# Performance work log

Hardware: AMD Instinct MI355X
Metric: run time of the kernel (lower is better)

The kernel has to match this reference:

```python
import jax, jax.numpy as jnp
import numpy as np

B, M, N = 4, 1024, 4096
DQ, DC, H, DH = 512, 512, 8, 64
D = H * DH
NEG = -10000000.0


def setup_inputs() -> dict:
    key = jax.random.key(0)
    ks = jax.random.split(key, 7)
    left = jax.random.normal(ks[0], (B, M, DQ), dtype=jnp.float32)
    right = jax.random.normal(ks[1], (B, N, DC), dtype=jnp.float32)
    mask = jax.random.randint(ks[2], (B, M, N), 0, 2).astype(bool)
    # learned params (torch Linear stores weight as (out,in); we store (in,out))
    Wq = jax.random.normal(ks[3], (DQ, D), dtype=jnp.float32) * (DQ ** -0.5)
    Wkv = jax.random.normal(ks[4], (DC, 2 * D), dtype=jnp.float32) * (DC ** -0.5)
    Wout = jax.random.normal(ks[5], (D, DQ), dtype=jnp.float32) * (D ** -0.5)
    bout = jax.random.normal(ks[6], (DQ,), dtype=jnp.float32) * 0.01
    return {"left": left, "right": right, "mask": mask,
            "Wq": Wq, "Wkv": Wkv, "Wout": Wout, "bout": bout}


def reference(left, right, mask, Wq, Wkv, Wout, bout):
    scale = DH ** -0.5
    q = left @ Wq                      # (B, M, D)
    kv = right @ Wkv                   # (B, N, 2D)
    k, v = jnp.split(kv, 2, axis=-1)   # (B, N, D) each
    q = q.reshape(B, M, H, DH).transpose(0, 2, 1, 3)  # (B, H, M, DH)
    k = k.reshape(B, N, H, DH).transpose(0, 2, 1, 3)  # (B, H, N, DH)
    v = v.reshape(B, N, H, DH).transpose(0, 2, 1, 3)  # (B, H, N, DH)
    sim = scale * jnp.einsum('bhmd,bhnd->bhmn', q, k)  # (B, H, M, N)
    sim = jnp.where(mask[:, None, :, :], sim, NEG)
    attn = jax.nn.softmax(sim, axis=-1)
    out = jnp.einsum('bhmn,bhnd->bhmd', attn, v)       # (B, H, M, DH)
    out = out.transpose(0, 2, 1, 3).reshape(B, M, D)
    return out @ Wout + bout           # (B, M, DQ)
```

## Files before the change

### kernel.cpp

```cpp
#include <hip/hip_runtime.h>

typedef _Float16 f16;
typedef __attribute__((ext_vector_type(8))) _Float16 half8;
typedef __attribute__((ext_vector_type(4))) _Float16 half4;
typedef __attribute__((ext_vector_type(4))) float floatx4;
typedef unsigned int uint32;

#define MFMA16(a, b, c) __builtin_amdgcn_mfma_f32_16x16x32_f16((a), (b), (c), 0, 0, 0)

constexpr int B_ = 4, M_ = 1024, N_ = 4096, DQ_ = 512, DC_ = 512, H_ = 8, DH_ = 64, D_ = 512;
constexpr int KP_ = 576;
constexpr int VP_ = 4224;
constexpr int NSPLIT = 4;
constexpr float SCL_ = 0.125f;

typedef __attribute__((address_space(1))) const void glds_g;
typedef __attribute__((address_space(3))) void glds_l;
__device__ __forceinline__ void g2lds16(const void* g, void* l) {
    __builtin_amdgcn_global_load_lds((glds_g*)g, (glds_l*)l, 16, 0, 0);
}

__device__ __forceinline__ void wtr_tile(const float* __restrict__ src, f16* __restrict__ dst,
                                         int Nout, int bx, int by, int tid) {
    __shared__ __align__(16) f16 Ts[64][72];
    const int n0 = bx * 64, k0 = by * 64;
    {
        int kr = tid >> 2, q4 = tid & 3;
        const float* sp = src + (size_t)(k0 + kr) * Nout + n0 + q4 * 16;
        float4 x0 = *(const float4*)(sp + 0), x1 = *(const float4*)(sp + 4);
        float4 x2 = *(const float4*)(sp + 8), x3 = *(const float4*)(sp + 12);
        half8 h0, h1;
        h0[0]=(f16)x0.x; h0[1]=(f16)x0.y; h0[2]=(f16)x0.z; h0[3]=(f16)x0.w;
        h0[4]=(f16)x1.x; h0[5]=(f16)x1.y; h0[6]=(f16)x1.z; h0[7]=(f16)x1.w;
        h1[0]=(f16)x2.x; h1[1]=(f16)x2.y; h1[2]=(f16)x2.z; h1[3]=(f16)x2.w;
        h1[4]=(f16)x3.x; h1[5]=(f16)x3.y; h1[6]=(f16)x3.z; h1[7]=(f16)x3.w;
        *(half8*)&Ts[kr][q4 * 16] = h0;
        *(half8*)&Ts[kr][q4 * 16 + 8] = h1;
    }
    __syncthreads();
    {
        int nr = tid >> 2, q = tid & 3;
        half8 h0, h1;
#pragma unroll
        for (int j = 0; j < 8; j++) { h0[j] = Ts[q * 16 + j][nr]; h1[j] = Ts[q * 16 + 8 + j][nr]; }
        f16* dp = dst + (size_t)(n0 + nr) * 512 + k0 + q * 16;
        *(half8*)(dp + 0) = h0;
        *(half8*)(dp + 8) = h1;
    }
}

__global__ __launch_bounds__(256)
void prep_k(const void* __restrict__ mask, uint32* __restrict__ bits,
            const float* __restrict__ left, f16* __restrict__ leftb,
            const float* __restrict__ right, f16* __restrict__ rightb,
            const float* __restrict__ Wq, f16* __restrict__ wqt,
            const float* __restrict__ Wkv, f16* __restrict__ wkvt,
            const float* __restrict__ Wout, f16* __restrict__ woutt) {
    const int blk = blockIdx.x, tid = threadIdx.x;
    if (blk < 4096) {
        __shared__ int s_bad;
        if (tid == 0) s_bad = 0;
        __syncthreads();
        const uint32* w = (const uint32*)mask + (size_t)blk * 1024;
        int bad = 0;
#pragma unroll
        for (int j = 0; j < 4; j++) bad |= (w[tid * 4 + j] & 0xFFFFFFFEu) != 0u;
        if (bad) s_bad = 1;
        __syncthreads();
        const bool bytes_mode = s_bad != 0;
        const size_t base = (size_t)blk * 4096;
        const int lane = tid & 63;
        for (int j = 0; j < 16; j++) {
            size_t e = base + j * 256 + tid;
            bool pred = bytes_mode ? (((const unsigned char*)mask)[e] != 0)
                                   : (((const int*)mask)[e] != 0);
            unsigned long long bal = __ballot(pred);
            if (lane == 0)       bits[e >> 5] = (uint32)bal;
            else if (lane == 32) bits[e >> 5] = (uint32)(bal >> 32);
        }
    } else if (blk < 6144) {
        int i = ((blk - 4096) * 256 + tid) * 4;
        float4 x = *(const float4*)(left + i);
        half4 h; h[0] = (f16)x.x; h[1] = (f16)x.y; h[2] = (f16)x.z; h[3] = (f16)x.w;
        *(half4*)(leftb + i) = h;
    } else if (blk < 14336) {
        int i = ((blk - 6144) * 256 + tid) * 4;
        float4 x = *(const float4*)(right + i);
        half4 h; h[0] = (f16)x.x; h[1] = (f16)x.y; h[2] = (f16)x.z; h[3] = (f16)x.w;
        *(half4*)(rightb + i) = h;
    } else if (blk < 14400) {
        int r = blk - 14336;
        wtr_tile(Wq, wqt, 512, r & 7, r >> 3, tid);
    } else if (blk < 14528) {
        int r = blk - 14400;
        wtr_tile(Wkv, wkvt, 1024, r & 15, r >> 4, tid);
    } else {
        int r = blk - 14528;
        wtr_tile(Wout, woutt, 512, r & 7, r >> 3, tid);
    }
}

__global__ __launch_bounds__(256)
void gemmqkv_k(const f16* __restrict__ leftb, const f16* __restrict__ wqt,
               const f16* __restrict__ rightb, const f16* __restrict__ wkvt,
               f16* __restrict__ qb, f16* __restrict__ kb, f16* __restrict__ vt) {
    __shared__ __align__(16) f16 As[128 * 64];
    __shared__ __align__(16) f16 Bs[128 * 64];
    const int blk = blockIdx.x, tid = threadIdx.x;
    const int lane = tid & 63, wave = tid >> 6;
    const int qd = lane >> 4, l16 = lane & 15;
    const int wm = wave >> 1, wn = wave & 1;

    int mode;
    const f16* A; const f16* Bt; size_t m0, n0;
    if (blk < 1024) {
        size_t rows = (size_t)(blk & 127) * 128, cols = (size_t)(blk >> 7) * 128;
        if (cols < 512) { mode = 0; A = rightb; m0 = rows; Bt = wkvt;   n0 = cols; }
        else            { mode = 1; A = wkvt;   m0 = cols; Bt = rightb; n0 = rows; }
    } else {
        int r = blk - 1024;
        mode = 2; A = leftb; Bt = wqt;
        m0 = (size_t)(r & 31) * 128; n0 = (size_t)(r >> 5) * 128;
    }

    size_t goff[4];
    f16 *la[4], *lb[4];
#pragma unroll
    for (int i = 0; i < 4; i++) {
        int c = i * 256 + wave * 64 + lane;
        int row = c >> 3, col8 = (c & 7) ^ (row & 7);
        goff[i] = (size_t)row * 512 + col8 * 8;
        la[i] = As + (size_t)(i * 256 + wave * 64) * 8;
        lb[i] = Bs + (size_t)(i * 256 + wave * 64) * 8;
    }
    const f16* Ab = A + m0 * 512;
    const f16* Bb = Bt + n0 * 512;

    floatx4 acc[4][4] = {};

    for (int k0 = 0; k0 < 512; k0 += 64) {
        __syncthreads();
#pragma unroll
        for (int i = 0; i < 4; i++) g2lds16(Ab + goff[i] + k0, la[i]);
#pragma unroll
        for (int i = 0; i < 4; i++) g2lds16(Bb + goff[i] + k0, lb[i]);
        __syncthreads();
#pragma unroll
        for (int kk = 0; kk < 2; kk++) {
            half8 a[4], b[4];
#pragma unroll
            for (int t = 0; t < 4; t++) {
                int rowa = wm * 64 + t * 16 + l16;
                int rowb = wn * 64 + t * 16 + l16;
                int pa8 = ((kk * 4 + qd) ^ (rowa & 7)) * 8;
                int pb8 = ((kk * 4 + qd) ^ (rowb & 7)) * 8;
                a[t] = *(const half8*)&As[rowa * 64 + pa8];
                b[t] = *(const half8*)&Bs[rowb * 64 + pb8];
            }
#pragma unroll
            for (int mt = 0; mt < 4; mt++)
#pragma unroll
                for (int nt = 0; nt < 4; nt++)
                    acc[mt][nt] = MFMA16(a[mt], b[nt], acc[mt][nt]);
        }
    }

#pragma unroll
    for (int mt = 0; mt < 4; mt++)
#pragma unroll
        for (int nt = 0; nt < 4; nt++)
#pragma unroll
            for (int r = 0; r < 4; r++) {
                size_t mi = m0 + wm * 64 + mt * 16 + qd * 4 + r;
                size_t ni = n0 + wn * 64 + nt * 16 + l16;
                float v = acc[mt][nt][r];
                if (mode == 2) {
                    qb[mi * 512 + ni] = (f16)v;
                } else if (mode == 0) {
                    kb[mi * KP_ + ni] = (f16)v;
                } else {
                    int dcol = (int)mi - 512;
                    int hh = dcol >> 6, dh = dcol & 63;
                    size_t bb = ni >> 12, nn = ni & 4095;
                    vt[((bb * H_ + hh) * (size_t)DH_ + dh) * VP_ + nn] = (f16)v;
                }
            }
}

__global__ __launch_bounds__(256)
void attn_k(const f16* __restrict__ Qb, const f16* __restrict__ Kb,
            const f16* __restrict__ Vt, const uint32* __restrict__ mb,
            float* __restrict__ Op, float* __restrict__ Lp) {
    const int tid = threadIdx.x;
    const int lane = tid & 63, wave = tid >> 6;
    const int qd = lane >> 4, l16 = lane & 15;
    const int bh = blockIdx.x, b = bh >> 3, h = bh & 7;
    const int z = blockIdx.z;
    constexpr int iters = N_ / (64 * NSPLIT);
    const int n_base = z * iters * 64;
    const int m_base = blockIdx.y * 128 + wave * 32;

    __shared__ __align__(16) f16 Ks[64][72];
    __shared__ __align__(16) f16 Vs[64][72];
    __shared__ __align__(16) f16 psh[4][32][72];

    const f16 scl = (f16)SCL_;
    half8 q[2][2];
#pragma unroll
    for (int f = 0; f < 2; f++) {
        const f16* qrow = Qb + ((size_t)(b * M_ + m_base + f * 16 + l16)) * D_ + h * DH_;
        q[f][0] = *(const half8*)(qrow + qd * 8);
        q[f][1] = *(const half8*)(qrow + 32 + qd * 8);
#pragma unroll
        for (int j = 0; j < 8; j++) { q[f][0][j] = q[f][0][j] * scl; q[f][1][j] = q[f][1][j] * scl; }
    }
    const half8 ONE = {(f16)1, (f16)1, (f16)1, (f16)1, (f16)1, (f16)1, (f16)1, (f16)1};

    floatx4 ot[2][4] = {};
    floatx4 ol[2] = {};
    const uint32* mbase = mb + ((size_t)(b * M_ + m_base)) * (N_ / 32);

    const int snr = tid >> 2, scc = tid & 3;
    const f16* kg = Kb + ((size_t)(b * N_) + snr) * KP_ + h * DH_ + scc * 8;
    const f16* vg = Vt + ((size_t)bh * DH_ + snr) * VP_ + scc * 8;

    for (int it = 0; it < iters; it++) {
        const int n0 = n_base + it * 64;
        half8 kc0 = *(const half8*)(kg + (size_t)n0 * KP_);
        half8 kc1 = *(const half8*)(kg + (size_t)n0 * KP_ + 32);
        half8 vc0 = *(const half8*)(vg + n0);
        half8 vc1 = *(const half8*)(vg + n0 + 32);
        __syncthreads();
        *(half8*)&Ks[snr][scc * 8]      = kc0;
        *(half8*)&Ks[snr][32 + scc * 8] = kc1;
        *(half8*)&Vs[snr][scc * 8]      = vc0;
        *(half8*)&Vs[snr][32 + scc * 8] = vc1;
        __syncthreads();

        const int wi = n0 >> 5;
        uint32 msk[2][4][2];
#pragma unroll
        for (int f = 0; f < 2; f++)
#pragma unroll
            for (int r = 0; r < 4; r++) {
                const uint32* mr = mbase + (size_t)(f * 16 + qd * 4 + r) * (N_ / 32);
                uint2 mm = *(const uint2*)(mr + wi);
                msk[f][r][0] = mm.x >> l16;
                msk[f][r][1] = mm.y >> l16;
            }

#pragma unroll
        for (int s = 0; s < 4; s++) {
            half8 k0 = *(const half8*)&Ks[s * 16 + l16][qd * 8];
            half8 k1 = *(const half8*)&Ks[s * 16 + l16][32 + qd * 8];
#pragma unroll
            for (int f = 0; f < 2; f++) {
                floatx4 t = {};
                t = MFMA16(q[f][0], k0, t);
                t = MFMA16(q[f][1], k1, t);
#pragma unroll
                for (int r = 0; r < 4; r++) {
                    uint32 bit = (msk[f][r][s >> 1] >> ((s & 1) * 16)) & 1u;
                    float e = __expf(t[r]);
                    e = bit ? e : 0.0f;
                    psh[wave][f * 16 + qd * 4 + r][s * 16 + l16] = (f16)e;
                }
            }
        }
        half8 pa[2][2];
#pragma unroll
        for (int f = 0; f < 2; f++) {
            pa[f][0] = *(const half8*)&psh[wave][f * 16 + l16][qd * 8];
            pa[f][1] = *(const half8*)&psh[wave][f * 16 + l16][32 + qd * 8];
        }
#pragma unroll
        for (int f = 0; f < 2; f++) {
            ol[f] = MFMA16(ONE, pa[f][0], ol[f]);
            ol[f] = MFMA16(ONE, pa[f][1], ol[f]);
        }
#pragma unroll
        for (int sd = 0; sd < 4; sd++) {
            half8 v0 = *(const half8*)&Vs[sd * 16 + l16][qd * 8];
            half8 v1 = *(const half8*)&Vs[sd * 16 + l16][32 + qd * 8];
#pragma unroll
            for (int f = 0; f < 2; f++) {
                ot[f][sd] = MFMA16(v0, pa[f][0], ot[f][sd]);
                ot[f][sd] = MFMA16(v1, pa[f][1], ot[f][sd]);
            }
        }
    }

#pragma unroll
    for (int f = 0; f < 2; f++) {
        size_t row = (size_t)(z * 32 + bh) * M_ + m_base + f * 16 + l16;
        float* op = Op + row * DH_ + qd * 4;
#pragma unroll
        for (int sd = 0; sd < 4; sd++)
            *(floatx4*)(op + sd * 16) = ot[f][sd];
        if (qd == 0) Lp[row] = ol[f][0];
    }
}

__global__ __launch_bounds__(256)
void comb_k(const float* __restrict__ Op, const float* __restrict__ Lp, f16* __restrict__ Ob) {
    int i = blockIdx.x * 256 + threadIdx.x;
    int d = i & 63, m = (i >> 6) & 1023, bh = i >> 16;
    float num = 0.f, den = 0.f;
#pragma unroll
    for (int s = 0; s < NSPLIT; s++) {
        size_t row = ((size_t)s * 32 + bh) * M_ + m;
        num += Op[row * DH_ + d];
        den += Lp[row];
    }
    int b = bh >> 3, h = bh & 7;
    Ob[((size_t)(b * M_ + m)) * D_ + h * DH_ + d] = (f16)(num / den);
}

__global__ __launch_bounds__(256)
void gemmout_k(const f16* __restrict__ A, const f16* __restrict__ Bt,
               float* __restrict__ Fout, const float* __restrict__ bias) {
    __shared__ __align__(16) f16 As[128 * 32];
    __shared__ __align__(16) f16 Bs[128 * 32];
    const int tid = threadIdx.x;
    const int lane = tid & 63, wave = tid >> 6;
    const int qd = lane >> 4, l16 = lane & 15;
    const int wm = wave >> 1, wn = wave & 1;
    const size_t m0 = (size_t)blockIdx.x * 128;
    const size_t n0 = (size_t)blockIdx.y * 128;

    const int c1 = wave * 64 + lane;
    const int c2 = 256 + c1;
    f16* la1 = As + (size_t)(wave * 64) * 8;
    f16* la2 = As + (size_t)(256 + wave * 64) * 8;
    f16* lb1 = Bs + (size_t)(wave * 64) * 8;
    f16* lb2 = Bs + (size_t)(256 + wave * 64) * 8;

    floatx4 acc[4][4] = {};

    for (int k0 = 0; k0 < 512; k0 += 32) {
        __syncthreads();
        g2lds16(A + (m0 + (c1 >> 2)) * 512 + k0 + (c1 & 3) * 8, la1);
        g2lds16(A + (m0 + (c2 >> 2)) * 512 + k0 + (c2 & 3) * 8, la2);
        g2lds16(Bt + (n0 + (c1 >> 2)) * 512 + k0 + (c1 & 3) * 8, lb1);
        g2lds16(Bt + (n0 + (c2 >> 2)) * 512 + k0 + (c2 & 3) * 8, lb2);
        __syncthreads();
        half8 a[4], b[4];
#pragma unroll
        for (int t = 0; t < 4; t++) {
            a[t] = *(const half8*)&As[(wm * 64 + t * 16 + l16) * 32 + qd * 8];
            b[t] = *(const half8*)&Bs[(wn * 64 + t * 16 + l16) * 32 + qd * 8];
        }
#pragma unroll
        for (int mt = 0; mt < 4; mt++)
#pragma unroll
            for (int nt = 0; nt < 4; nt++)
                acc[mt][nt] = MFMA16(a[mt], b[nt], acc[mt][nt]);
    }

#pragma unroll
    for (int mt = 0; mt < 4; mt++)
#pragma unroll
        for (int nt = 0; nt < 4; nt++)
#pragma unroll
            for (int r = 0; r < 4; r++) {
                size_t row = m0 + wm * 64 + mt * 16 + qd * 4 + r;
                size_t col = n0 + wn * 64 + nt * 16 + l16;
                Fout[row * 512 + col] = acc[mt][nt][r] + bias[col];
            }
}

extern "C" void kernel_launch(void* const* d_in, const int* in_sizes, int n_in,
                              void* d_out, int out_size, void* d_ws, size_t ws_size,
                              hipStream_t stream) {
    const float* left  = (const float*)d_in[0];
    const float* right = (const float*)d_in[1];
    const void*  mask  = d_in[2];
    const float* Wq    = (const float*)d_in[3];
    const float* Wkv   = (const float*)d_in[4];
    const float* Wout  = (const float*)d_in[5];
    const float* bout  = (const float*)d_in[6];

    char* ws = (char*)d_ws;
    size_t off = 0;
    auto take = [&](size_t bytes) { char* p = ws + off; off += (bytes + 255) & ~(size_t)255; return p; };
    uint32* mbits = (uint32*)take((size_t)B_ * M_ * N_ / 8);
    f16* woutt = (f16*)take((size_t)D_ * DQ_ * 2);
    f16* qb    = (f16*)take((size_t)B_ * M_ * D_ * 2);
    f16* kb    = (f16*)take((size_t)B_ * N_ * KP_ * 2);
    f16* vt    = (f16*)take((size_t)B_ * H_ * DH_ * VP_ * 2);
    f16* ob    = (f16*)take((size_t)B_ * M_ * D_ * 2);
    char* pool = (char*)take((size_t)34 * 1024 * 1024);
    f16* leftb  = (f16*)pool;
    f16* rightb = (f16*)(pool + (size_t)4 * 1024 * 1024);
    f16* wqt    = (f16*)(pool + (size_t)20 * 1024 * 1024);
    f16* wkvt   = (f16*)(pool + (size_t)21 * 1024 * 1024);
    float* Op   = (float*)pool;
    float* Lp   = (float*)(pool + (size_t)NSPLIT * 32 * M_ * DH_ * 4);

    prep_k<<<14592, 256, 0, stream>>>(mask, mbits, left, leftb, right, rightb,
                                      Wq, wqt, Wkv, wkvt, Wout, woutt);
    gemmqkv_k<<<1152, 256, 0, stream>>>(leftb, wqt, rightb, wkvt, qb, kb, vt);
    attn_k<<<dim3(32, 8, NSPLIT), 256, 0, stream>>>(qb, kb, vt, mbits, Op, Lp);
    comb_k<<<8192, 256, 0, stream>>>(Op, Lp, ob);
    gemmout_k<<<dim3(32, 4), 256, 0, stream>>>(ob, woutt, (float*)d_out, bout);
}
```

Baseline: 281.5 us.

## Rework attention inner loop: direct LDS loads, register P transpose, exp2, more splits

K and V tiles now go straight from global memory into XOR-swizzled LDS through global_load_lds, which removes the register staging step. The QK^T MFMA operands are swapped so that each lane holds a row fragment. That fragment is then rebuilt into the PV operand with permlane32/16 swaps, so the per-wave P shared-memory round trip is gone. The softmax uses exp2 with log2(e) folded into the Q scale and packs results with cvt_pkrtz. The split count becomes 8 when the workspace is large enough, with an occupancy hint, and the combine kernel is vectorized to float4. This adds split-combine traffic, and permlane correctness depends on the lane layout.

```diff
diff --git a/kernel.cpp b/kernel.cpp
--- a/kernel.cpp
+++ b/kernel.cpp
@@ -5,14 +5,14 @@
 typedef __attribute__((ext_vector_type(4))) _Float16 half4;
 typedef __attribute__((ext_vector_type(4))) float floatx4;
 typedef unsigned int uint32;
+typedef __attribute__((ext_vector_type(4))) uint32 uint4v;
 
 #define MFMA16(a, b, c) __builtin_amdgcn_mfma_f32_16x16x32_f16((a), (b), (c), 0, 0, 0)
 
 constexpr int B_ = 4, M_ = 1024, N_ = 4096, DQ_ = 512, DC_ = 512, H_ = 8, DH_ = 64, D_ = 512;
 constexpr int KP_ = 576;
 constexpr int VP_ = 4224;
-constexpr int NSPLIT = 4;
-constexpr float SCL_ = 0.125f;
+constexpr float QSC_ = 0.18033688011112042f;
 
 typedef __attribute__((address_space(1))) const void glds_g;
 typedef __attribute__((address_space(3))) void glds_l;
@@ -187,7 +187,7 @@
             }
 }
 
-__global__ __launch_bounds__(256)
+__global__ __launch_bounds__(256, 6)
 void attn_k(const f16* __restrict__ Qb, const f16* __restrict__ Kb,
             const f16* __restrict__ Vt, const uint32* __restrict__ mb,
             float* __restrict__ Op, float* __restrict__ Lp) {
@@ -195,84 +195,102 @@
     const int lane = tid & 63, wave = tid >> 6;
     const int qd = lane >> 4, l16 = lane & 15;
     const int bh = blockIdx.x, b = bh >> 3, h = bh & 7;
-    const int z = blockIdx.z;
-    constexpr int iters = N_ / (64 * NSPLIT);
+    const int z = blockIdx.z, nsp = gridDim.z;
+    const int iters = N_ / (64 * nsp);
     const int n_base = z * iters * 64;
     const int m_base = blockIdx.y * 128 + wave * 32;
 
-    __shared__ __align__(16) f16 Ks[64][72];
-    __shared__ __align__(16) f16 Vs[64][72];
-    __shared__ __align__(16) f16 psh[4][32][72];
-
-    const f16 scl = (f16)SCL_;
+    __shared__ __align__(16) f16 Ks[64 * 64];
+    __shared__ __align__(16) f16 Vs[64 * 64];
+
     half8 q[2][2];
 #pragma unroll
     for (int f = 0; f < 2; f++) {
         const f16* qrow = Qb + ((size_t)(b * M_ + m_base + f * 16 + l16)) * D_ + h * DH_;
-        q[f][0] = *(const half8*)(qrow + qd * 8);
-        q[f][1] = *(const half8*)(qrow + 32 + qd * 8);
-#pragma unroll
-        for (int j = 0; j < 8; j++) { q[f][0][j] = q[f][0][j] * scl; q[f][1][j] = q[f][1][j] * scl; }
+        half8 r0 = *(const half8*)(qrow + qd * 8);
+        half8 r1 = *(const half8*)(qrow + 32 + qd * 8);
+#pragma unroll
+        for (int j = 0; j < 8; j++) {
+            q[f][0][j] = (f16)((float)r0[j] * QSC_);
+            q[f][1][j] = (f16)((float)r1[j] * QSC_);
+        }
     }
     const half8 ONE = {(f16)1, (f16)1, (f16)1, (f16)1, (f16)1, (f16)1, (f16)1, (f16)1};
 
     floatx4 ot[2][4] = {};
     floatx4 ol[2] = {};
-    const uint32* mbase = mb + ((size_t)(b * M_ + m_base)) * (N_ / 32);
-
-    const int snr = tid >> 2, scc = tid & 3;
-    const f16* kg = Kb + ((size_t)(b * N_) + snr) * KP_ + h * DH_ + scc * 8;
-    const f16* vg = Vt + ((size_t)bh * DH_ + snr) * VP_ + scc * 8;
+
+    const uint32* mrow0 = mb + ((size_t)(b * M_ + m_base + l16)) * (N_ / 32);
+    const uint32* mrow1 = mrow0 + (size_t)16 * (N_ / 32);
+
+    const int srow = wave * 16;
+    const int r8 = lane >> 3, p8 = lane & 7;
+    const int gc8 = p8 ^ r8;
+    const f16* kg = Kb + ((size_t)(b * N_) + srow + r8) * KP_ + h * DH_ + gc8 * 8;
+    const f16* vg = Vt + ((size_t)(bh * DH_) + srow + r8) * VP_ + gc8 * 8;
+    const int sw = (l16 & 7) * 8;
 
     for (int it = 0; it < iters; it++) {
         const int n0 = n_base + it * 64;
-        half8 kc0 = *(const half8*)(kg + (size_t)n0 * KP_);
-        half8 kc1 = *(const half8*)(kg + (size_t)n0 * KP_ + 32);
-        half8 vc0 = *(const half8*)(vg + n0);
-        half8 vc1 = *(const half8*)(vg + n0 + 32);
-        __syncthreads();
-        *(half8*)&Ks[snr][scc * 8]      = kc0;
-        *(half8*)&Ks[snr][32 + scc * 8] = kc1;
-        *(half8*)&Vs[snr][scc * 8]      = vc0;
-        *(half8*)&Vs[snr][32 + scc * 8] = vc1;
-        __syncthreads();
-
-        const int wi = n0 >> 5;
-        uint32 msk[2][4][2];
-#pragma unroll
-        for (int f = 0; f < 2; f++)
-#pragma unroll
-            for (int r = 0; r < 4; r++) {
-                const uint32* mr = mbase + (size_t)(f * 16 + qd * 4 + r) * (N_ / 32);
-                uint2 mm = *(const uint2*)(mr + wi);
-                msk[f][r][0] = mm.x >> l16;
-                msk[f][r][1] = mm.y >> l16;
-            }
-
+        __syncthreads();
+#pragma unroll
+        for (int j = 0; j < 2; j++) {
+            g2lds16(kg + ((size_t)n0 + j * 8) * KP_, Ks + (srow + j * 8) * 64);
+            g2lds16(vg + (size_t)(j * 8) * VP_ + n0, Vs + (srow + j * 8) * 64);
+        }
+        uint2 mm0 = *(const uint2*)(mrow0 + (n0 >> 5));
+        uint2 mm1 = *(const uint2*)(mrow1 + (n0 >> 5));
+        __syncthreads();
+
+        uint32 u[2][2] = {{mm0.x >> (qd * 4), mm0.y >> (qd * 4)},
+                          {mm1.x >> (qd * 4), mm1.y >> (qd * 4)}};
+
+        uint32 pk[2][4][2];
 #pragma unroll
         for (int s = 0; s < 4; s++) {
-            half8 k0 = *(const half8*)&Ks[s * 16 + l16][qd * 8];
-            half8 k1 = *(const half8*)&Ks[s * 16 + l16][32 + qd * 8];
+            const int ro = (s * 16 + l16) * 64;
+            half8 k0 = *(const half8*)&Ks[ro + (((qd) ^ (l16 & 7)) * 8)];
+            half8 k1 = *(const half8*)&Ks[ro + (((4 + qd) ^ (l16 & 7)) * 8)];
 #pragma unroll
             for (int f = 0; f < 2; f++) {
                 floatx4 t = {};
-                t = MFMA16(q[f][0], k0, t);
-                t = MFMA16(q[f][1], k1, t);
-#pragma unroll
-                for (int r = 0; r < 4; r++) {
-                    uint32 bit = (msk[f][r][s >> 1] >> ((s & 1) * 16)) & 1u;
-                    float e = __expf(t[r]);
-                    e = bit ? e : 0.0f;
-                    psh[wave][f * 16 + qd * 4 + r][s * 16 + l16] = (f16)e;
+                t = MFMA16(k0, q[f][0], t);
+                t = MFMA16(k1, q[f][1], t);
+                uint32 us = u[f][s >> 1] >> ((s & 1) * 16);
+                float e0 = __builtin_amdgcn_exp2f(t[0]);
+                float e1 = __builtin_amdgcn_exp2f(t[1]);
+                float e2 = __builtin_amdgcn_exp2f(t[2]);
+                float e3 = __builtin_amdgcn_exp2f(t[3]);
+                e0 = (us & 1u) ? e0 : 0.0f;
+                e1 = (us & 2u) ? e1 : 0.0f;
+                e2 = (us & 4u) ? e2 : 0.0f;
+                e3 = (us & 8u) ? e3 : 0.0f;
+                pk[f][s][0] = __builtin_bit_cast(uint32, __builtin_amdgcn_cvt_pkrtz(e0, e1));
+                pk[f][s][1] = __builtin_bit_cast(uint32, __builtin_amdgcn_cvt_pkrtz(e2, e3));
+            }
+        }
+
+        half8 pa[2][2];
+#pragma unroll
+        for (int f = 0; f < 2; f++) {
+#pragma unroll
+            for (int hh = 0; hh < 2; hh++) {
+                uint32 w0, w1, w2, w3;
+                {
+                    auto a = __builtin_amdgcn_permlane32_swap(pk[f][2 * hh][0], pk[f][2 * hh + 1][0], false, false);
+                    auto c = __builtin_amdgcn_permlane16_swap(a[0], a[1], false, false);
+                    w0 = c[0]; w2 = c[1];
                 }
-            }
-        }
-        half8 pa[2][2];
-#pragma unroll
-        for (int f = 0; f < 2; f++) {
-            pa[f][0] = *(const half8*)&psh[wave][f * 16 + l16][qd * 8];
-            pa[f][1] = *(const half8*)&psh[wave][f * 16 + l16][32 + qd * 8];
-        }
+                {
+                    auto a = __builtin_amdgcn_permlane32_swap(pk[f][2 * hh][1], pk[f][2 * hh + 1][1], false, false);
+                    auto c = __builtin_amdgcn_permlane16_swap(a[0], a[1], false, false);
+                    w1 = c[0]; w3 = c[1];
+                }
+                uint4v wv = {w0, w1, w2, w3};
+                pa[f][hh] = __builtin_bit_cast(half8, wv);
+            }
+        }
+
 #pragma unroll
         for (int f = 0; f < 2; f++) {
             ol[f] = MFMA16(ONE, pa[f][0], ol[f]);
@@ -280,8 +298,9 @@
         }
 #pragma unroll
         for (int sd = 0; sd < 4; sd++) {
-            half8 v0 = *(const half8*)&Vs[sd * 16 + l16][qd * 8];
-            half8 v1 = *(const half8*)&Vs[sd * 16 + l16][32 + qd * 8];
+            const int ro = (sd * 16 + l16) * 64;
+            half8 v0 = *(const half8*)&Vs[ro + (((qd) ^ (l16 & 7)) * 8)];
+            half8 v1 = *(const half8*)&Vs[ro + (((4 + qd) ^ (l16 & 7)) * 8)];
 #pragma unroll
             for (int f = 0; f < 2; f++) {
                 ot[f][sd] = MFMA16(v0, pa[f][0], ot[f][sd]);
@@ -302,18 +321,22 @@
 }
 
 __global__ __launch_bounds__(256)
-void comb_k(const float* __restrict__ Op, const float* __restrict__ Lp, f16* __restrict__ Ob) {
+void comb_k(const float* __restrict__ Op, const float* __restrict__ Lp, f16* __restrict__ Ob,
+            int nsp) {
     int i = blockIdx.x * 256 + threadIdx.x;
-    int d = i & 63, m = (i >> 6) & 1023, bh = i >> 16;
-    float num = 0.f, den = 0.f;
-#pragma unroll
-    for (int s = 0; s < NSPLIT; s++) {
+    int d4 = i & 15, m = (i >> 4) & 1023, bh = i >> 14;
+    float nx = 0.f, ny = 0.f, nz = 0.f, nw = 0.f, den = 0.f;
+    for (int s = 0; s < nsp; s++) {
         size_t row = ((size_t)s * 32 + bh) * M_ + m;
-        num += Op[row * DH_ + d];
+        float4 x = *(const float4*)(Op + row * DH_ + d4 * 4);
+        nx += x.x; ny += x.y; nz += x.z; nw += x.w;
         den += Lp[row];
     }
+    float r = 1.0f / den;
     int b = bh >> 3, h = bh & 7;
-    Ob[((size_t)(b * M_ + m)) * D_ + h * DH_ + d] = (f16)(num / den);
+    f16* o = Ob + ((size_t)(b * M_ + m)) * D_ + h * DH_ + d4 * 4;
+    half4 hv; hv[0] = (f16)(nx * r); hv[1] = (f16)(ny * r); hv[2] = (f16)(nz * r); hv[3] = (f16)(nw * r);
+    *(half4*)o = hv;
 }
 
 __global__ __launch_bounds__(256)
@@ -389,18 +412,25 @@
     f16* kb    = (f16*)take((size_t)B_ * N_ * KP_ * 2);
     f16* vt    = (f16*)take((size_t)B_ * H_ * DH_ * VP_ * 2);
     f16* ob    = (f16*)take((size_t)B_ * M_ * D_ * 2);
-    char* pool = (char*)take((size_t)34 * 1024 * 1024);
+    char* pool = ws + off;
+    const size_t op1 = (size_t)32 * M_ * DH_ * 4;
+    const size_t lp1 = (size_t)32 * M_ * 4;
+    const size_t phase1 = (size_t)22 * 1024 * 1024;
+    size_t p8 = 8 * (op1 + lp1);
+    size_t need8 = off + (p8 > phase1 ? p8 : phase1);
+    const int nsp = (ws_size >= need8) ? 8 : 4;
+
     f16* leftb  = (f16*)pool;
     f16* rightb = (f16*)(pool + (size_t)4 * 1024 * 1024);
     f16* wqt    = (f16*)(pool + (size_t)20 * 1024 * 1024);
     f16* wkvt   = (f16*)(pool + (size_t)21 * 1024 * 1024);
     float* Op   = (float*)pool;
-    float* Lp   = (float*)(pool + (size_t)NSPLIT * 32 * M_ * DH_ * 4);
+    float* Lp   = (float*)(pool + (size_t)nsp * op1);
 
     prep_k<<<14592, 256, 0, stream>>>(mask, mbits, left, leftb, right, rightb,
                                       Wq, wqt, Wkv, wkvt, Wout, woutt);
     gemmqkv_k<<<1152, 256, 0, stream>>>(leftb, wqt, rightb, wkvt, qb, kb, vt);
-    attn_k<<<dim3(32, 8, NSPLIT), 256, 0, stream>>>(qb, kb, vt, mbits, Op, Lp);
-    comb_k<<<8192, 256, 0, stream>>>(Op, Lp, ob);
+    attn_k<<<dim3(32, 8, nsp), 256, 0, stream>>>(qb, kb, vt, mbits, Op, Lp);
+    comb_k<<<2048, 256, 0, stream>>>(Op, Lp, ob, nsp);
     gemmout_k<<<dim3(32, 4), 256, 0, stream>>>(ob, woutt, (float*)d_out, bout);
 }
```

New measurement: 358.8 us. 27.4% more time.
